# Kernel optimization log

Measured on AMD Instinct MI355X. Metric: run time of the kernel, lower is better.

Reference implementation:

```python
import jax, jax.numpy as jnp
import numpy as np

BN_EPS = 1e-5


def setup_inputs() -> dict:
    key = jax.random.key(0)
    ks = jax.random.split(key, 9)
    b, c, h, w = 8, 256, 256, 25
    p2_r = jax.random.normal(ks[0], (b, c, h, w), dtype=jnp.float32)
    # message-passing conv weight; scaled so the 25-step recurrence stays bounded
    W_msg = jax.random.normal(ks[1], (256, 256, 1, 9), dtype=jnp.float32) * 0.02
    bn_gamma = jax.random.uniform(ks[2], (256,), dtype=jnp.float32, minval=0.5, maxval=1.5)
    bn_beta = jax.random.normal(ks[3], (256,), dtype=jnp.float32) * 0.1
    bn_mean = jax.random.normal(ks[4], (256,), dtype=jnp.float32) * 0.1
    bn_var = jax.random.uniform(ks[5], (256,), dtype=jnp.float32, minval=0.5, maxval=1.5)
    W_up2 = jax.random.normal(ks[6], (256, 256, 3, 3), dtype=jnp.float32) * (1.0 / np.sqrt(256 * 9))
    W_conv = jax.random.normal(ks[7], (1, 256, 1, 1), dtype=jnp.float32) * (1.0 / np.sqrt(256))
    W_conv2 = jax.random.normal(ks[8], (1, 25, 1, 1), dtype=jnp.float32) * (1.0 / np.sqrt(25))
    return {"p2_r": p2_r, "W_msg": W_msg, "bn_gamma": bn_gamma, "bn_beta": bn_beta,
            "bn_mean": bn_mean, "bn_var": bn_var, "W_up2": W_up2,
            "W_conv": W_conv, "W_conv2": W_conv2}


def r_scnn(x, Wc, reverse):
    # x: [b,c,h,w]. The (1,9) conv with padding (0,4) on width-1 slices only
    # touches the kernel's center tap -> per-step 256x256 matvec recurrence.
    xs = jnp.moveaxis(x, 3, 0)  # [w,b,c,h]
    if reverse:
        xs = xs[::-1]

    def step(carry, xi):
        new = xi + jax.nn.relu(jnp.einsum('oc,bch->boh', Wc, carry))
        return new, new

    _, rest = jax.lax.scan(step, xs[0], xs[1:])
    out = jnp.concatenate([xs[:1], rest], axis=0)[::-1]  # source reverses output order
    return jnp.moveaxis(out, 0, 3)  # [b,c,h,w]


def batchnorm(x, gamma, beta, mean, var):
    inv = gamma / jnp.sqrt(var + BN_EPS)
    return x * inv[None, :, None, None] + (beta - mean * inv)[None, :, None, None]


def upsample_h2(x):
    # bilinear, align_corners=True, size=(2H, W): only height doubles
    b, c, H, W = x.shape
    nh = 2 * H
    pos = jnp.arange(nh, dtype=jnp.float32) * ((H - 1) / (nh - 1))
    i0 = jnp.floor(pos).astype(jnp.int32)
    i1 = jnp.minimum(i0 + 1, H - 1)
    t = (pos - i0.astype(jnp.float32))[None, None, :, None]
    return x[:, :, i0, :] * (1.0 - t) + x[:, :, i1, :] * t


def reference(p2_r, W_msg, bn_gamma, bn_beta, bn_mean, bn_var, W_up2, W_conv, W_conv2):
    Wc = W_msg[:, :, 0, 4]  # effective center tap of the (1,9) conv
    x = r_scnn(p2_r, Wc, reverse=False)
    x = jax.nn.relu(batchnorm(x, bn_gamma, bn_beta, bn_mean, bn_var))
    x = r_scnn(x, Wc, reverse=True)
    x = jax.nn.relu(batchnorm(x, bn_gamma, bn_beta, bn_mean, bn_var))
    x = upsample_h2(x)  # [b,256,2h,w]
    x = jax.lax.conv_general_dilated(x, W_up2, (1, 1), ((1, 1), (1, 1)),
                                     dimension_numbers=('NCHW', 'OIHW', 'NCHW'))
    x = upsample_h2(x)  # [b,256,4h,w]
    x = jnp.einsum('oc,bchw->bohw', W_conv[:, :, 0, 0], x)  # 1x1 conv 256->1
    x = upsample_h2(x)  # [b,1,8h,w]
    x = jnp.swapaxes(x, 1, 3)  # [b,w,8h,1]
    x = jnp.einsum('oc,bchw->bohw', W_conv2[:, :, 0, 0], x)  # 1x1 conv 25->1
    return jax.nn.sigmoid(x)  # [b,1,8h,1]
```

## Files before the change

### kernel.cpp

```cpp
#include <hip/hip_runtime.h>
#include <math.h>


#define NC 8

typedef __attribute__((ext_vector_type(8))) short bf16x8;
typedef __attribute__((ext_vector_type(4))) float f32x4;

__device__ __forceinline__ float relu_(float v) { return fmaxf(v, 0.f); }

__device__ __forceinline__ short f2bf(float f) {
  union { float f; unsigned u; } v; v.f = f;
  unsigned r = (v.u + 0x7fffu + ((v.u >> 16) & 1u)) >> 16;
  return (short)r;
}
__device__ __forceinline__ float bf2f(short s) {
  union { unsigned u; float f; } v;
  v.u = ((unsigned)(unsigned short)s) << 16;
  return v.f;
}

__global__ __launch_bounds__(64) void k0_precompute(
    const float* __restrict__ Wmsg, const float* __restrict__ gamma,
    const float* __restrict__ beta, const float* __restrict__ mean,
    const float* __restrict__ var, const float* __restrict__ Wup2,
    const float* __restrict__ Wconv, const float* __restrict__ Wconv2,
    short* __restrict__ WcA, float* __restrict__ A, float* __restrict__ bnp)
{
  const int c = blockIdx.x;
  const int lane = threadIdx.x;

  for (int o = lane; o < 256; o += 64)
    WcA[o * 256 + c] = f2bf(Wmsg[(o * 256 + c) * 9 + 4]);

  const int gtid = c * 64 + lane;
  if (gtid < 256) {
    float inv = gamma[gtid] / sqrtf(var[gtid] + 1e-5f);
    bnp[gtid] = inv;
    bnp[256 + gtid] = beta[gtid] - mean[gtid] * inv;
  }

  float wacc[9];
#pragma unroll
  for (int q = 0; q < 9; ++q) wacc[q] = 0.f;
  for (int o = lane; o < 256; o += 64) {
    float cw = Wconv[o];
    const float* wp = Wup2 + (size_t)(o * 256 + c) * 9;
#pragma unroll
    for (int q = 0; q < 9; ++q) wacc[q] += cw * wp[q];
  }
#pragma unroll
  for (int q = 0; q < 9; ++q) {
    float v = wacc[q];
    v += __shfl_xor(v, 32, 64);
    v += __shfl_xor(v, 16, 64);
    v += __shfl_xor(v, 8, 64);
    v += __shfl_xor(v, 4, 64);
    v += __shfl_xor(v, 2, 64);
    v += __shfl_xor(v, 1, 64);
    wacc[q] = v;
  }
  if (lane == 0) {
    for (int dh = 0; dh < 3; ++dh)
      for (int j = 0; j < 25; ++j) {
        float a = 0.f;
        for (int dw = 0; dw < 3; ++dw) {
          int w = j + 1 - dw;
          if (w >= 0 && w < 25) a += wacc[dh * 3 + dw] * Wconv2[w];
        }
        A[(dh * 25 + j) * 256 + c] = a;
      }
  }
}

__global__ __launch_bounds__(512) void k2_fused(
    const float* __restrict__ X,
    const short* __restrict__ WcA,
    const float* __restrict__ A,
    const float* __restrict__ bnp,
    float* __restrict__ S)
{
  __shared__ short xslab[25 * 8 * 256];
  __shared__ short yz[2][16 * 256];
  __shared__ float red[8][8][3];
  const int tid = threadIdx.x;
  const int wave = tid >> 6;
  const int lane = tid & 63;
  const int n = lane & 15;
  const int nr = n & 7;
  const int g = lane >> 4;
  const bool isz = (n >= 8);
  const int col0 = blockIdx.x * NC;
  const int b = col0 >> 8, h0 = col0 & 255;
  const int obase = wave * 32;
  char* xs = (char*)xslab;
  char* smem = (char*)yz;

  {
    const int c = tid >> 1;
    const int half = tid & 1;
    const float* src = X + ((size_t)(b * 256 + c) * 256 + h0) * 25 + half * 100;
#pragma unroll
    for (int j = 0; j < 25; ++j) {
      float4 v = *(const float4*)(src + j * 4);
      int f0 = half * 100 + j * 4;
      float vv[4] = {v.x, v.y, v.z, v.w};
#pragma unroll
      for (int e = 0; e < 4; ++e) {
        int f = f0 + e;
        int rn = f / 25;
        int w = f - rn * 25;
        *(short*)(xs + w * 4096 + rn * 512 + ((2 * c) ^ (rn << 4))) = f2bf(vv[e]);
      }
    }
  }

  f32x4 inv[2], addv[2];
#pragma unroll
  for (int t = 0; t < 2; ++t) {
    inv[t] = *(const f32x4*)(bnp + obase + t * 16 + g * 4);
    addv[t] = *(const f32x4*)(bnp + 256 + obase + t * 16 + g * 4);
  }

  bf16x8 af[2][8];
#pragma unroll
  for (int t = 0; t < 2; ++t)
#pragma unroll
    for (int kk = 0; kk < 8; ++kk)
      af[t][kk] = *(const bf16x8*)(WcA + (obase + t * 16 + n) * 256 + kk * 32 + g * 8);

  const int swz = nr << 4;
  int woff[2], roff[8], xoff[2];
#pragma unroll
  for (int t = 0; t < 2; ++t) {
    woff[t] = n * 512 + (((obase + t * 16 + g * 4) * 2) ^ swz);
    xoff[t] = nr * 512 + (((obase + t * 16 + g * 4) * 2) ^ swz);
  }
#pragma unroll
  for (int kk = 0; kk < 8; ++kk)
    roff[kk] = n * 512 + ((kk * 64 + g * 16) ^ swz);

  float sA0 = 0.f, sA1 = 0.f, sA2 = 0.f;

  __syncthreads();

  {
    f32x4 a4[3][2];
#pragma unroll
    for (int dh = 0; dh < 3; ++dh)
#pragma unroll
      for (int t = 0; t < 2; ++t) a4[dh][t] = (f32x4){0.f, 0.f, 0.f, 0.f};
    if (isz) {
#pragma unroll
      for (int dh = 0; dh < 3; ++dh)
#pragma unroll
        for (int t = 0; t < 2; ++t)
          a4[dh][t] = *(const f32x4*)(A + (dh * 25 + 24) * 256 + obase + t * 16 + g * 4);
    }
    short vp[2][4];
#pragma unroll
    for (int t = 0; t < 2; ++t) {
      uint2 q = *(const uint2*)(xs + xoff[t]);
      short xb[4] = {(short)(q.x), (short)(q.x >> 16), (short)(q.y), (short)(q.y >> 16)};
#pragma unroll
      for (int r = 0; r < 4; ++r) {
        float v = bf2f(xb[r]);
        if (isz) v = relu_(v * inv[t][r] + addv[t][r]);
        float t2 = relu_(v * inv[t][r] + addv[t][r]);
        sA0 = fmaf(a4[0][t][r], t2, sA0);
        sA1 = fmaf(a4[1][t][r], t2, sA1);
        sA2 = fmaf(a4[2][t][r], t2, sA2);
        vp[t][r] = f2bf(v);
      }
    }
#pragma unroll
    for (int t = 0; t < 2; ++t)
      *(short4*)(smem + woff[t]) = make_short4(vp[t][0], vp[t][1], vp[t][2], vp[t][3]);
  }

  f32x4 aN[3][2];
#pragma unroll
  for (int dh = 0; dh < 3; ++dh)
#pragma unroll
    for (int t = 0; t < 2; ++t) aN[dh][t] = (f32x4){0.f, 0.f, 0.f, 0.f};
  if (isz) {
#pragma unroll
    for (int dh = 0; dh < 3; ++dh)
#pragma unroll
      for (int t = 0; t < 2; ++t)
        aN[dh][t] = *(const f32x4*)(A + (dh * 25 + 23) * 256 + obase + t * 16 + g * 4);
  }
  __syncthreads();

#pragma unroll 1
  for (int k = 1; k < 25; ++k) {
    const int cur = (k - 1) & 1, nxt = k & 1;

    bf16x8 bfr[8];
#pragma unroll
    for (int kk = 0; kk < 8; ++kk)
      bfr[kk] = *(const bf16x8*)(smem + cur * 8192 + roff[kk]);
    uint2 xq[2];
    xq[0] = make_uint2(0u, 0u);
    xq[1] = make_uint2(0u, 0u);
    if (!isz) {
#pragma unroll
      for (int t = 0; t < 2; ++t)
        xq[t] = *(const uint2*)(xs + k * 4096 + xoff[t]);
    }

    f32x4 aC[3][2];
#pragma unroll
    for (int dh = 0; dh < 3; ++dh)
#pragma unroll
      for (int t = 0; t < 2; ++t) aC[dh][t] = aN[dh][t];
    if (isz && k < 24) {
      const int wn = 23 - k;
#pragma unroll
      for (int dh = 0; dh < 3; ++dh)
#pragma unroll
        for (int t = 0; t < 2; ++t)
          aN[dh][t] = *(const f32x4*)(A + (dh * 25 + wn) * 256 + obase + t * 16 + g * 4);
    }

    f32x4 acc0a = (f32x4){0.f, 0.f, 0.f, 0.f};
    f32x4 acc0b = (f32x4){0.f, 0.f, 0.f, 0.f};
    f32x4 acc1a = (f32x4){0.f, 0.f, 0.f, 0.f};
    f32x4 acc1b = (f32x4){0.f, 0.f, 0.f, 0.f};
#pragma unroll
    for (int kk = 0; kk < 4; ++kk) {
      acc0a = __builtin_amdgcn_mfma_f32_16x16x32_bf16(af[0][kk], bfr[kk], acc0a, 0, 0, 0);
      acc1a = __builtin_amdgcn_mfma_f32_16x16x32_bf16(af[1][kk], bfr[kk], acc1a, 0, 0, 0);
    }
#pragma unroll
    for (int kk = 4; kk < 8; ++kk) {
      acc0b = __builtin_amdgcn_mfma_f32_16x16x32_bf16(af[0][kk], bfr[kk], acc0b, 0, 0, 0);
      acc1b = __builtin_amdgcn_mfma_f32_16x16x32_bf16(af[1][kk], bfr[kk], acc1b, 0, 0, 0);
    }
    f32x4 acc0 = acc0a + acc0b;
    f32x4 acc1 = acc1a + acc1b;

    short vp[2][4];
#pragma unroll
    for (int t = 0; t < 2; ++t) {
      f32x4 acc = t ? acc1 : acc0;
      short xb[4] = {(short)(xq[t].x), (short)(xq[t].x >> 16),
                     (short)(xq[t].y), (short)(xq[t].y >> 16)};
#pragma unroll
      for (int r = 0; r < 4; ++r) {
        float cy = relu_(acc[r]);
        float ynew = bf2f(xb[r]) + cy;
        float t1 = relu_(ynew * inv[t][r] + addv[t][r]);
        float t1s = __shfl_xor(t1, 8);
        float znew = t1s + cy;
        float t2 = relu_(znew * inv[t][r] + addv[t][r]);
        sA0 = fmaf(aC[0][t][r], t2, sA0);
        sA1 = fmaf(aC[1][t][r], t2, sA1);
        sA2 = fmaf(aC[2][t][r], t2, sA2);
        vp[t][r] = f2bf(isz ? znew : ynew);
      }
    }
#pragma unroll
    for (int t = 0; t < 2; ++t)
      *(short4*)(smem + nxt * 8192 + woff[t]) =
          make_short4(vp[t][0], vp[t][1], vp[t][2], vp[t][3]);
    __syncthreads();
  }

  sA0 += __shfl_xor(sA0, 16); sA0 += __shfl_xor(sA0, 32);
  sA1 += __shfl_xor(sA1, 16); sA1 += __shfl_xor(sA1, 32);
  sA2 += __shfl_xor(sA2, 16); sA2 += __shfl_xor(sA2, 32);
  if (isz && g == 0) {
    red[wave][n - 8][0] = sA0;
    red[wave][n - 8][1] = sA1;
    red[wave][n - 8][2] = sA2;
  }
  __syncthreads();
  if (tid < 24) {
    int nn = tid / 3, dh = tid % 3;
    float v = 0.f;
#pragma unroll
    for (int ww = 0; ww < 8; ++ww) v += red[ww][nn][dh];
    S[(size_t)(col0 + nn) * 3 + dh] = v;
  }
}

__global__ __launch_bounds__(256) void k3_outpre(
    const float* __restrict__ S, float* __restrict__ P)
{
  int idx = blockIdx.x * blockDim.x + threadIdx.x;
  if (idx >= 8 * 512) return;
  int b = idx >> 9, h = idx & 511;
  float acc = 0.f;
#pragma unroll
  for (int dh = 0; dh < 3; ++dh) {
    int hh = h + dh - 1;
    if (hh < 0 || hh >= 512) continue;
    float pos = hh * (255.0f / 511.0f);
    int i0 = (int)floorf(pos);
    int i1 = min(i0 + 1, 255);
    float t = pos - (float)i0;
    acc += (1.f - t) * S[(size_t)(b * 256 + i0) * 3 + dh]
         + t * S[(size_t)(b * 256 + i1) * 3 + dh];
  }
  P[idx] = acc;
}

__global__ __launch_bounds__(256) void k4_final(
    const float* __restrict__ P, float* __restrict__ out)
{
  int idx = blockIdx.x * blockDim.x + threadIdx.x;
  if (idx >= 8 * 2048) return;
  int b = idx >> 11, H = idx & 2047;
  const float* Pb = P + b * 512;

  float pos3 = H * (1023.0f / 2047.0f);
  int i3 = (int)floorf(pos3);
  int i3b = min(i3 + 1, 1023);
  float t3 = pos3 - (float)i3;

  float v[2];
#pragma unroll
  for (int q = 0; q < 2; ++q) {
    int i = q ? i3b : i3;
    float pos2 = i * (511.0f / 1023.0f);
    int i2 = (int)floorf(pos2);
    int i2b = min(i2 + 1, 511);
    float t2 = pos2 - (float)i2;
    v[q] = (1.f - t2) * Pb[i2] + t2 * Pb[i2b];
  }
  float val = (1.f - t3) * v[0] + t3 * v[1];
  out[idx] = 1.f / (1.f + expf(-val));
}

extern "C" void kernel_launch(void* const* d_in, const int* in_sizes, int n_in,
                              void* d_out, int out_size, void* d_ws, size_t ws_size,
                              hipStream_t stream) {
  (void)in_sizes; (void)n_in; (void)out_size; (void)ws_size;
  const float* p2r    = (const float*)d_in[0];
  const float* Wmsg   = (const float*)d_in[1];
  const float* gamma  = (const float*)d_in[2];
  const float* beta   = (const float*)d_in[3];
  const float* mean   = (const float*)d_in[4];
  const float* var    = (const float*)d_in[5];
  const float* Wup2   = (const float*)d_in[6];
  const float* Wconv  = (const float*)d_in[7];
  const float* Wconv2 = (const float*)d_in[8];
  float* out = (float*)d_out;

  float* ws = (float*)d_ws;
  size_t off = 0;
  short* WcA = (short*)(ws + off); off += 32768;
  float* Abuf = ws + off; off += 19200;
  float* bnp = ws + off;  off += 512;
  float* S = ws + off;    off += 6144;
  float* P = ws + off;    off += 4096;

  k0_precompute<<<256, 64, 0, stream>>>(Wmsg, gamma, beta, mean, var, Wup2,
                                        Wconv, Wconv2, WcA, Abuf, bnp);
  k2_fused<<<256, 512, 0, stream>>>(p2r, (const short*)WcA, Abuf, bnp, S);
  k3_outpre<<<16, 256, 0, stream>>>(S, P);
  k4_final<<<64, 256, 0, stream>>>(P, out);
}
```

Baseline: 60.14 us.

## Defer A-weighted reduction out of recurrence loop via LDS stash of activations

The per-step FMA reduction against A weights is taken out of the serial 24-step recurrence. Each step's z activations are written back in bf16 into the now-free x slab, and after the loop all threads do the reduction with coalesced A loads and shuffle trees. The change also drops the XOR swizzle on the x slab, splits input staging across 512 threads, and packs bf16 with v_cvt_pk_bf16_f32. This shortens the latency-critical loop and removes the per-step global A prefetch. The cost is a post-loop pass, possible LDS bank conflicts without the swizzle, and the stored t2 values being rounded to bf16.

```diff
diff --git a/kernel.cpp b/kernel.cpp
--- a/kernel.cpp
+++ b/kernel.cpp
@@ -18,6 +18,11 @@
   union { unsigned u; float f; } v;
   v.u = ((unsigned)(unsigned short)s) << 16;
   return v.f;
+}
+__device__ __forceinline__ unsigned cvtpk(float lo, float hi) {
+  unsigned r;
+  asm("v_cvt_pk_bf16_f32 %0, %1, %2" : "=v"(r) : "v"(lo), "v"(hi));
+  return r;
 }
 
 __global__ __launch_bounds__(64) void k0_precompute(
@@ -97,21 +102,24 @@
   char* smem = (char*)yz;
 
   {
-    const int c = tid >> 1;
-    const int half = tid & 1;
-    const float* src = X + ((size_t)(b * 256 + c) * 256 + h0) * 25 + half * 100;
-#pragma unroll
-    for (int j = 0; j < 25; ++j) {
-      float4 v = *(const float4*)(src + j * 4);
-      int f0 = half * 100 + j * 4;
-      float vv[4] = {v.x, v.y, v.z, v.w};
-#pragma unroll
-      for (int e = 0; e < 4; ++e) {
-        int f = f0 + e;
-        int rn = f / 25;
-        int w = f - rn * 25;
-        *(short*)(xs + w * 4096 + rn * 512 + ((2 * c) ^ (rn << 4))) = f2bf(vv[e]);
-      }
+    auto stage = [&](int cc, const float* src, int fbase) {
+#pragma unroll
+      for (int j = 0; j < 25; ++j) {
+        float4 v = *(const float4*)(src + j * 4);
+        float vv[4] = {v.x, v.y, v.z, v.w};
+#pragma unroll
+        for (int e = 0; e < 4; ++e) {
+          int f = fbase + j * 4 + e;
+          int rn = f / 25, w = f - rn * 25;
+          *(short*)(xs + w * 4096 + rn * 512 + 2 * cc) = f2bf(vv[e]);
+        }
+      }
+    };
+    if (tid < 256) {
+      stage(tid, X + ((size_t)(b * 256 + tid) * 256 + h0) * 25, 0);
+    } else {
+      int c2 = tid - 256;
+      stage(c2, X + ((size_t)(b * 256 + c2) * 256 + h0) * 25 + 100, 100);
     }
   }
 
@@ -134,61 +142,38 @@
 #pragma unroll
   for (int t = 0; t < 2; ++t) {
     woff[t] = n * 512 + (((obase + t * 16 + g * 4) * 2) ^ swz);
-    xoff[t] = nr * 512 + (((obase + t * 16 + g * 4) * 2) ^ swz);
+    xoff[t] = nr * 512 + 2 * (obase + t * 16 + g * 4);
   }
 #pragma unroll
   for (int kk = 0; kk < 8; ++kk)
     roff[kk] = n * 512 + ((kk * 64 + g * 16) ^ swz);
 
-  float sA0 = 0.f, sA1 = 0.f, sA2 = 0.f;
-
   __syncthreads();
 
   {
-    f32x4 a4[3][2];
-#pragma unroll
-    for (int dh = 0; dh < 3; ++dh)
-#pragma unroll
-      for (int t = 0; t < 2; ++t) a4[dh][t] = (f32x4){0.f, 0.f, 0.f, 0.f};
-    if (isz) {
-#pragma unroll
-      for (int dh = 0; dh < 3; ++dh)
-#pragma unroll
-        for (int t = 0; t < 2; ++t)
-          a4[dh][t] = *(const f32x4*)(A + (dh * 25 + 24) * 256 + obase + t * 16 + g * 4);
-    }
-    short vp[2][4];
-#pragma unroll
-    for (int t = 0; t < 2; ++t) {
-      uint2 q = *(const uint2*)(xs + xoff[t]);
-      short xb[4] = {(short)(q.x), (short)(q.x >> 16), (short)(q.y), (short)(q.y >> 16)};
-#pragma unroll
-      for (int r = 0; r < 4; ++r) {
-        float v = bf2f(xb[r]);
-        if (isz) v = relu_(v * inv[t][r] + addv[t][r]);
-        float t2 = relu_(v * inv[t][r] + addv[t][r]);
-        sA0 = fmaf(a4[0][t][r], t2, sA0);
-        sA1 = fmaf(a4[1][t][r], t2, sA1);
-        sA2 = fmaf(a4[2][t][r], t2, sA2);
-        vp[t][r] = f2bf(v);
-      }
-    }
-#pragma unroll
-    for (int t = 0; t < 2; ++t)
-      *(short4*)(smem + woff[t]) = make_short4(vp[t][0], vp[t][1], vp[t][2], vp[t][3]);
-  }
-
-  f32x4 aN[3][2];
-#pragma unroll
-  for (int dh = 0; dh < 3; ++dh)
-#pragma unroll
-    for (int t = 0; t < 2; ++t) aN[dh][t] = (f32x4){0.f, 0.f, 0.f, 0.f};
-  if (isz) {
-#pragma unroll
-    for (int dh = 0; dh < 3; ++dh)
+    uint2 xq0[2];
+#pragma unroll
+    for (int t = 0; t < 2; ++t) xq0[t] = *(const uint2*)(xs + xoff[t]);
+    if (!isz) {
 #pragma unroll
       for (int t = 0; t < 2; ++t)
-        aN[dh][t] = *(const f32x4*)(A + (dh * 25 + 23) * 256 + obase + t * 16 + g * 4);
+        *(uint2*)(smem + woff[t]) = xq0[t];
+    } else {
+#pragma unroll
+      for (int t = 0; t < 2; ++t) {
+        float zr[4], t2r[4];
+#pragma unroll
+        for (int r = 0; r < 4; ++r) {
+          short xb = (short)(r < 2 ? (r ? (xq0[t].x >> 16) : xq0[t].x)
+                                   : (r & 1 ? (xq0[t].y >> 16) : xq0[t].y));
+          float x = bf2f(xb);
+          zr[r] = relu_(x * inv[t][r] + addv[t][r]);
+          t2r[r] = relu_(zr[r] * inv[t][r] + addv[t][r]);
+        }
+        *(uint2*)(smem + woff[t]) = make_uint2(cvtpk(zr[0], zr[1]), cvtpk(zr[2], zr[3]));
+        *(uint2*)(xs + xoff[t]) = make_uint2(cvtpk(t2r[0], t2r[1]), cvtpk(t2r[2], t2r[3]));
+      }
+    }
   }
   __syncthreads();
 
@@ -196,10 +181,6 @@
   for (int k = 1; k < 25; ++k) {
     const int cur = (k - 1) & 1, nxt = k & 1;
 
-    bf16x8 bfr[8];
-#pragma unroll
-    for (int kk = 0; kk < 8; ++kk)
-      bfr[kk] = *(const bf16x8*)(smem + cur * 8192 + roff[kk]);
     uint2 xq[2];
     xq[0] = make_uint2(0u, 0u);
     xq[1] = make_uint2(0u, 0u);
@@ -209,19 +190,10 @@
         xq[t] = *(const uint2*)(xs + k * 4096 + xoff[t]);
     }
 
-    f32x4 aC[3][2];
-#pragma unroll
-    for (int dh = 0; dh < 3; ++dh)
-#pragma unroll
-      for (int t = 0; t < 2; ++t) aC[dh][t] = aN[dh][t];
-    if (isz && k < 24) {
-      const int wn = 23 - k;
-#pragma unroll
-      for (int dh = 0; dh < 3; ++dh)
-#pragma unroll
-        for (int t = 0; t < 2; ++t)
-          aN[dh][t] = *(const f32x4*)(A + (dh * 25 + wn) * 256 + obase + t * 16 + g * 4);
-    }
+    bf16x8 bfr[8];
+#pragma unroll
+    for (int kk = 0; kk < 8; ++kk)
+      bfr[kk] = *(const bf16x8*)(smem + cur * 8192 + roff[kk]);
 
     f32x4 acc0a = (f32x4){0.f, 0.f, 0.f, 0.f};
     f32x4 acc0b = (f32x4){0.f, 0.f, 0.f, 0.f};
@@ -240,40 +212,69 @@
     f32x4 acc0 = acc0a + acc0b;
     f32x4 acc1 = acc1a + acc1b;
 
-    short vp[2][4];
 #pragma unroll
     for (int t = 0; t < 2; ++t) {
       f32x4 acc = t ? acc1 : acc0;
-      short xb[4] = {(short)(xq[t].x), (short)(xq[t].x >> 16),
-                     (short)(xq[t].y), (short)(xq[t].y >> 16)};
+      float xv[4];
+      xv[0] = bf2f((short)xq[t].x);
+      xv[1] = bf2f((short)(xq[t].x >> 16));
+      xv[2] = bf2f((short)xq[t].y);
+      xv[3] = bf2f((short)(xq[t].y >> 16));
+      float sel[4], tt2[4];
 #pragma unroll
       for (int r = 0; r < 4; ++r) {
         float cy = relu_(acc[r]);
-        float ynew = bf2f(xb[r]) + cy;
+        float ynew = xv[r] + cy;
         float t1 = relu_(ynew * inv[t][r] + addv[t][r]);
         float t1s = __shfl_xor(t1, 8);
         float znew = t1s + cy;
-        float t2 = relu_(znew * inv[t][r] + addv[t][r]);
-        sA0 = fmaf(aC[0][t][r], t2, sA0);
-        sA1 = fmaf(aC[1][t][r], t2, sA1);
-        sA2 = fmaf(aC[2][t][r], t2, sA2);
-        vp[t][r] = f2bf(isz ? znew : ynew);
-      }
-    }
-#pragma unroll
-    for (int t = 0; t < 2; ++t)
-      *(short4*)(smem + nxt * 8192 + woff[t]) =
-          make_short4(vp[t][0], vp[t][1], vp[t][2], vp[t][3]);
+        tt2[r] = relu_(znew * inv[t][r] + addv[t][r]);
+        sel[r] = isz ? znew : ynew;
+      }
+      *(uint2*)(smem + nxt * 8192 + woff[t]) =
+          make_uint2(cvtpk(sel[0], sel[1]), cvtpk(sel[2], sel[3]));
+      if (isz)
+        *(uint2*)(xs + k * 4096 + xoff[t]) =
+            make_uint2(cvtpk(tt2[0], tt2[1]), cvtpk(tt2[2], tt2[3]));
+    }
     __syncthreads();
   }
 
-  sA0 += __shfl_xor(sA0, 16); sA0 += __shfl_xor(sA0, 32);
-  sA1 += __shfl_xor(sA1, 16); sA1 += __shfl_xor(sA1, 32);
-  sA2 += __shfl_xor(sA2, 16); sA2 += __shfl_xor(sA2, 32);
-  if (isz && g == 0) {
-    red[wave][n - 8][0] = sA0;
-    red[wave][n - 8][1] = sA1;
-    red[wave][n - 8][2] = sA2;
+  {
+    const int c = tid & 255;
+    const int kh = tid >> 8;
+    float acc[8][3];
+#pragma unroll
+    for (int nn = 0; nn < 8; ++nn)
+#pragma unroll
+      for (int dh = 0; dh < 3; ++dh) acc[nn][dh] = 0.f;
+
+    const int kbeg = kh ? 13 : 0, kend = kh ? 25 : 13;
+    for (int k = kbeg; k < kend; ++k) {
+      float a0 = A[(0 * 25 + 24 - k) * 256 + c];
+      float a1 = A[(1 * 25 + 24 - k) * 256 + c];
+      float a2 = A[(2 * 25 + 24 - k) * 256 + c];
+#pragma unroll
+      for (int nn = 0; nn < 8; ++nn) {
+        float v = bf2f(*(const short*)(xs + k * 4096 + nn * 512 + 2 * c));
+        acc[nn][0] = fmaf(a0, v, acc[nn][0]);
+        acc[nn][1] = fmaf(a1, v, acc[nn][1]);
+        acc[nn][2] = fmaf(a2, v, acc[nn][2]);
+      }
+    }
+#pragma unroll
+    for (int nn = 0; nn < 8; ++nn)
+#pragma unroll
+      for (int dh = 0; dh < 3; ++dh) {
+        float v = acc[nn][dh];
+        v += __shfl_xor(v, 1);
+        v += __shfl_xor(v, 2);
+        v += __shfl_xor(v, 4);
+        v += __shfl_xor(v, 8);
+        v += __shfl_xor(v, 16);
+        v += __shfl_xor(v, 32);
+        if (lane == 0) red[wave][nn][dh] = v;
+      }
   }
   __syncthreads();
   if (tid < 24) {
```

After: 64.68 us. +7.5%, slower.
